# Kernel tuning notes

Measured on AMD Instinct MI355X. Metric: run time of the kernel, lower is better.

The kernel has to match this reference:

```python
import jax, jax.numpy as jnp
import numpy as np

B, HN, N1, N2, S = 32, 12, 256, 320, 256  # S = hardcoded 256 buffer size
EPS = 1e-5


def setup_inputs() -> dict:
    key = jax.random.key(0)
    ks = jax.random.split(key, 6)
    attn_rgb = jax.random.normal(ks[0], (B, HN, N1, N2), dtype=jnp.float32)
    attn_tir = jax.random.normal(ks[1], (B, HN, N1, N2), dtype=jnp.float32)
    # per-batch unique indices in [0, 256): permutation (collision-free scatter)
    perm = jax.vmap(lambda k: jax.random.permutation(k, S))(jax.random.split(ks[2], B))
    global_index_s = perm[:, :N1].astype(jnp.int32)
    # LayerNorm(512) params
    ln_g = jnp.ones((2 * S,), jnp.float32)
    ln_b = jnp.zeros((2 * S,), jnp.float32)
    # Linear(512,256) xavier-uniform weight, zero bias (stored as [in,out])
    lim1 = float(np.sqrt(6.0 / (2 * S + S)))
    W1 = jax.random.uniform(ks[3], (2 * S, S), jnp.float32, -lim1, lim1)
    b1 = jnp.zeros((S,), jnp.float32)
    # Linear(256,512)
    lim2 = float(np.sqrt(6.0 / (S + 2 * S)))
    W2 = jax.random.uniform(ks[4], (S, 2 * S), jnp.float32, -lim2, lim2)
    b2 = jnp.zeros((2 * S,), jnp.float32)
    return {"attn_rgb": attn_rgb, "attn_tir": attn_tir, "global_index_s": global_index_s,
            "ln_g": ln_g, "ln_b": ln_b, "W1": W1, "b1": b1, "W2": W2, "b2": b2}


def reference(attn_rgb, attn_tir, global_index_s, ln_g, ln_b, W1, b1, W2, b2):
    Bv, hn, n1, _ = attn_rgb.shape
    idx = jnp.broadcast_to(global_index_s[:, None, :].astype(jnp.int32), (Bv, hn, n1))  # [B,hn,N1]
    # detach() in torch source -> stop_gradient on the max-pooled path
    mx_rgb = jax.lax.stop_gradient(attn_rgb).max(-1)  # [B,hn,N1]
    mx_tir = jax.lax.stop_gradient(attn_tir).max(-1)
    bi = jnp.arange(Bv)[:, None, None]
    hi = jnp.arange(hn)[None, :, None]
    vex_rgb = jnp.zeros((Bv, hn, S), attn_rgb.dtype).at[bi, hi, idx].set(mx_rgb)
    vex_tir = jnp.zeros((Bv, hn, S), attn_tir.dtype).at[bi, hi, idx].set(mx_tir)
    v = jnp.concatenate([vex_rgb, vex_tir], axis=-1)  # [B,hn,512]
    # LayerNorm(512)
    mu = v.mean(-1, keepdims=True)
    var = v.var(-1, keepdims=True)
    v = (v - mu) * jax.lax.rsqrt(var + EPS) * ln_g + ln_b
    # SE MLP: Linear -> ReLU -> Linear -> Sigmoid
    h = jax.nn.relu(jnp.einsum('bhe,ef->bhf', v, W1) + b1)
    g = jax.nn.sigmoid(jnp.einsum('bhf,fe->bhe', h, W2) + b2)  # [B,hn,512]
    # gather gates back via indices and modulate
    g_rgb = jnp.take_along_axis(g[..., :S], idx, axis=-1)[..., None]  # [B,hn,N1,1]
    g_tir = jnp.take_along_axis(g[..., S:], idx, axis=-1)[..., None]
    attn_rgb_col = g_rgb * attn_rgb
    attn_tir_col = g_tir * attn_tir
    return (attn_tir_col, attn_rgb_col)
```

## Files before the change

### kernel.cpp

```cpp
#include <hip/hip_runtime.h>
#include <hip/hip_bf16.h>
#include <math.h>

#define BB   32
#define HN   12
#define N1   256
#define N2   320
#define SS   256
#define BH   (BB*HN)
#define R4   (N2/4)
#define SLICE4 ((size_t)N1*R4)

typedef float v4f __attribute__((ext_vector_type(4)));

__global__ __launch_bounds__(256, 2) void k_fused(
    const float* __restrict__ rgb, const float* __restrict__ tir,
    const int*   __restrict__ gidx,
    const float* __restrict__ ln_g, const float* __restrict__ ln_b,
    const float* __restrict__ W1,  const float* __restrict__ b1,
    const float* __restrict__ W2,  const float* __restrict__ b2,
    v4f* __restrict__ outTir, v4f* __restrict__ outRgb)
{
    __shared__ float mxs[2 * SS];
    __shared__ float v[2 * SS];
    __shared__ float hs[SS];
    __shared__ float gs[2 * SS];
    __shared__ float growR[SS];
    __shared__ float growT[SS];
    __shared__ int   sidx_s[SS];
    __shared__ float red[8];

    const int bh   = (int)blockIdx.x;
    const int b    = bh / HN;
    const int t    = (int)threadIdx.x;
    const int w    = t >> 6;
    const int lane = t & 63;

    sidx_s[t] = gidx[b * SS + t];
    v[t] = 0.f; v[t + SS] = 0.f;

    const v4f* srcR = (const v4f*)rgb + (size_t)bh * SLICE4;
    const v4f* srcT = (const v4f*)tir + (size_t)bh * SLICE4;

    for (int rr = 0; rr < 64; rr += 4) {
        const int r = w * 64 + rr;
        v4f aR[4], bRv[4], aT[4], bTv[4];
#pragma unroll
        for (int q = 0; q < 4; ++q) {
            const v4f* pR = srcR + (size_t)(r + q) * R4;
            const v4f* pT = srcT + (size_t)(r + q) * R4;
            aR[q]  = pR[lane];
            bRv[q] = pR[64 + (lane & 15)];
            aT[q]  = pT[lane];
            bTv[q] = pT[64 + (lane & 15)];
        }
#pragma unroll
        for (int q = 0; q < 4; ++q) {
            float mR = fmaxf(fmaxf(fmaxf(aR[q].x, aR[q].y), fmaxf(aR[q].z, aR[q].w)),
                             fmaxf(fmaxf(bRv[q].x, bRv[q].y), fmaxf(bRv[q].z, bRv[q].w)));
            float mT = fmaxf(fmaxf(fmaxf(aT[q].x, aT[q].y), fmaxf(aT[q].z, aT[q].w)),
                             fmaxf(fmaxf(bTv[q].x, bTv[q].y), fmaxf(bTv[q].z, bTv[q].w)));
#pragma unroll
            for (int off = 32; off; off >>= 1) {
                mR = fmaxf(mR, __shfl_xor(mR, off));
                mT = fmaxf(mT, __shfl_xor(mT, off));
            }
            if (lane == 0) { mxs[r + q] = mR; mxs[SS + r + q] = mT; }
        }
    }
    __syncthreads();

    {
        int sidx = sidx_s[t];
        v[sidx]      = mxs[t];
        v[sidx + SS] = mxs[SS + t];
    }
    __syncthreads();

    {
        float x0 = v[t], x1 = v[t + SS];
        float s  = x0 + x1;
        float sq = x0 * x0 + x1 * x1;
#pragma unroll
        for (int off = 32; off; off >>= 1) {
            s  += __shfl_xor(s, off);
            sq += __shfl_xor(sq, off);
        }
        if (lane == 0) { red[w] = s; red[4 + w] = sq; }
        __syncthreads();
        s  = red[0] + red[1] + red[2] + red[3];
        sq = red[4] + red[5] + red[6] + red[7];
        const float mu   = s * (1.f / 512.f);
        const float var  = sq * (1.f / 512.f) - mu * mu;
        const float rstd = rsqrtf(var + 1e-5f);
        v[t]      = (x0 - mu) * rstd * ln_g[t]      + ln_b[t];
        v[t + SS] = (x1 - mu) * rstd * ln_g[t + SS] + ln_b[t + SS];
    }
    __syncthreads();

    {
        float a0 = b1[t], a1 = 0.f;
#pragma unroll 8
        for (int e = 0; e < SS; ++e)       a0 = fmaf(v[e], W1[e * SS + t], a0);
#pragma unroll 8
        for (int e = SS; e < 2 * SS; ++e)  a1 = fmaf(v[e], W1[e * SS + t], a1);
        hs[t] = fmaxf(a0 + a1, 0.f);
    }
    __syncthreads();

    {
        float lo0 = b2[t], lo1 = 0.f, hi0 = b2[t + SS], hi1 = 0.f;
#pragma unroll 8
        for (int f = 0; f < 128; ++f) {
            float hv = hs[f];
            lo0 = fmaf(hv, W2[f * 2 * SS + t],      lo0);
            hi0 = fmaf(hv, W2[f * 2 * SS + t + SS], hi0);
        }
#pragma unroll 8
        for (int f = 128; f < SS; ++f) {
            float hv = hs[f];
            lo1 = fmaf(hv, W2[f * 2 * SS + t],      lo1);
            hi1 = fmaf(hv, W2[f * 2 * SS + t + SS], hi1);
        }
        gs[t]      = 1.f / (1.f + expf(-(lo0 + lo1)));
        gs[t + SS] = 1.f / (1.f + expf(-(hi0 + hi1)));
    }
    __syncthreads();

    growR[t] = gs[sidx_s[t]];
    growT[t] = gs[sidx_s[t] + SS];
    __syncthreads();

    {
        v4f* dstR = outRgb + (size_t)bh * SLICE4;
        v4f* dstT = outTir + (size_t)bh * SLICE4;
        for (int k = 0; k < 80; k += 8) {
            v4f aR[8], aT[8];
#pragma unroll
            for (int q = 0; q < 8; ++q) {
                unsigned i = (unsigned)(k + q) * 256u + (unsigned)t;
                aR[q] = srcR[i];
                aT[q] = srcT[i];
            }
#pragma unroll
            for (int q = 0; q < 8; ++q) {
                unsigned i   = (unsigned)(k + q) * 256u + (unsigned)t;
                unsigned row = i / 80u;
                v4f oR = aR[q] * growR[row];
                v4f oT = aT[q] * growT[row];
                __builtin_nontemporal_store(oT, dstT + i);
                __builtin_nontemporal_store(oR, dstR + i);
            }
        }
    }
}

extern "C" void kernel_launch(void* const* d_in, const int* in_sizes, int n_in,
                              void* d_out, int out_size, void* d_ws, size_t ws_size,
                              hipStream_t stream)
{
    const float* attn_rgb = (const float*)d_in[0];
    const float* attn_tir = (const float*)d_in[1];
    const int*   gidx     = (const int*)  d_in[2];
    const float* ln_g     = (const float*)d_in[3];
    const float* ln_b     = (const float*)d_in[4];
    const float* W1       = (const float*)d_in[5];
    const float* b1       = (const float*)d_in[6];
    const float* W2       = (const float*)d_in[7];
    const float* b2       = (const float*)d_in[8];

    v4f* outTir = (v4f*)d_out;
    v4f* outRgb = outTir + (size_t)BH * SLICE4;

    k_fused<<<BH, 256, 0, stream>>>(attn_rgb, attn_tir, gidx, ln_g, ln_b,
                                    W1, b1, W2, b2, outTir, outRgb);
}
```

Before: 138.9 us.

## Split fused kernel into rowmax, MLP, and modulate kernels for wider parallelism

Replaces the single per-(batch,head) fused kernel with three kernels: a grid-wide row-max reduction, a small per-(batch,head) LayerNorm+MLP kernel writing gate rows to workspace, and a wide elementwise modulation kernel. The goal is to fill the GPU with many more blocks during the two bandwidth-bound passes instead of 384 large blocks. It adds two kernel launches, a serial MLP stage between the passes, and workspace round-trips for maxima and gates.

```diff
diff --git a/kernel.cpp b/kernel.cpp
--- a/kernel.cpp
+++ b/kernel.cpp
@@ -8,25 +8,63 @@
 #define N2   320
 #define SS   256
 #define BH   (BB*HN)
+#define ROWS (BH*N1)
 #define R4   (N2/4)
-#define SLICE4 ((size_t)N1*R4)
+#define N4PT ((size_t)ROWS*R4)
 
 typedef float v4f __attribute__((ext_vector_type(4)));
 
-__global__ __launch_bounds__(256, 2) void k_fused(
+#define K1_BLOCKS 2048
+#define K1_WAVES  (K1_BLOCKS*4)
+#define ROWS_TOTAL (2*ROWS)
+#define RPW (ROWS_TOTAL/K1_WAVES)
+
+__global__ __launch_bounds__(256) void k_rowmax(
     const float* __restrict__ rgb, const float* __restrict__ tir,
+    float* __restrict__ mxr, float* __restrict__ mxt)
+{
+    const int gw   = ((int)blockIdx.x * 256 + (int)threadIdx.x) >> 6;
+    const int lane = threadIdx.x & 63;
+    const int base = gw * RPW;
+
+    for (int rr = 0; rr < RPW; rr += 4) {
+        v4f a[4], b[4];
+#pragma unroll
+        for (int q = 0; q < 4; ++q) {
+            int row   = base + rr + q;
+            int isTir = row >= ROWS;
+            int r     = isTir ? row - ROWS : row;
+            const v4f* p = (const v4f*)((isTir ? tir : rgb) + (size_t)r * N2);
+            a[q] = p[lane];
+            b[q] = p[64 + (lane & 15)];
+        }
+#pragma unroll
+        for (int q = 0; q < 4; ++q) {
+            float m = fmaxf(fmaxf(fmaxf(a[q].x, a[q].y), fmaxf(a[q].z, a[q].w)),
+                            fmaxf(fmaxf(b[q].x, b[q].y), fmaxf(b[q].z, b[q].w)));
+#pragma unroll
+            for (int off = 32; off; off >>= 1) m = fmaxf(m, __shfl_xor(m, off));
+            if (lane == 0) {
+                int row   = base + rr + q;
+                int isTir = row >= ROWS;
+                int r     = isTir ? row - ROWS : row;
+                (isTir ? mxt : mxr)[r] = m;
+            }
+        }
+    }
+}
+
+__global__ __launch_bounds__(256) void k_mlp(
     const int*   __restrict__ gidx,
+    const float* __restrict__ mxr, const float* __restrict__ mxt,
     const float* __restrict__ ln_g, const float* __restrict__ ln_b,
     const float* __restrict__ W1,  const float* __restrict__ b1,
     const float* __restrict__ W2,  const float* __restrict__ b2,
-    v4f* __restrict__ outTir, v4f* __restrict__ outRgb)
+    float* __restrict__ growR, float* __restrict__ growT)
 {
-    __shared__ float mxs[2 * SS];
     __shared__ float v[2 * SS];
     __shared__ float hs[SS];
     __shared__ float gs[2 * SS];
-    __shared__ float growR[SS];
-    __shared__ float growT[SS];
     __shared__ int   sidx_s[SS];
     __shared__ float red[8];
 
@@ -38,42 +76,12 @@
 
     sidx_s[t] = gidx[b * SS + t];
     v[t] = 0.f; v[t + SS] = 0.f;
-
-    const v4f* srcR = (const v4f*)rgb + (size_t)bh * SLICE4;
-    const v4f* srcT = (const v4f*)tir + (size_t)bh * SLICE4;
-
-    for (int rr = 0; rr < 64; rr += 4) {
-        const int r = w * 64 + rr;
-        v4f aR[4], bRv[4], aT[4], bTv[4];
-#pragma unroll
-        for (int q = 0; q < 4; ++q) {
-            const v4f* pR = srcR + (size_t)(r + q) * R4;
-            const v4f* pT = srcT + (size_t)(r + q) * R4;
-            aR[q]  = pR[lane];
-            bRv[q] = pR[64 + (lane & 15)];
-            aT[q]  = pT[lane];
-            bTv[q] = pT[64 + (lane & 15)];
-        }
-#pragma unroll
-        for (int q = 0; q < 4; ++q) {
-            float mR = fmaxf(fmaxf(fmaxf(aR[q].x, aR[q].y), fmaxf(aR[q].z, aR[q].w)),
-                             fmaxf(fmaxf(bRv[q].x, bRv[q].y), fmaxf(bRv[q].z, bRv[q].w)));
-            float mT = fmaxf(fmaxf(fmaxf(aT[q].x, aT[q].y), fmaxf(aT[q].z, aT[q].w)),
-                             fmaxf(fmaxf(bTv[q].x, bTv[q].y), fmaxf(bTv[q].z, bTv[q].w)));
-#pragma unroll
-            for (int off = 32; off; off >>= 1) {
-                mR = fmaxf(mR, __shfl_xor(mR, off));
-                mT = fmaxf(mT, __shfl_xor(mT, off));
-            }
-            if (lane == 0) { mxs[r + q] = mR; mxs[SS + r + q] = mT; }
-        }
-    }
     __syncthreads();
 
     {
         int sidx = sidx_s[t];
-        v[sidx]      = mxs[t];
-        v[sidx + SS] = mxs[SS + t];
+        v[sidx]      = mxr[bh * N1 + t];
+        v[sidx + SS] = mxt[bh * N1 + t];
     }
     __syncthreads();
 
@@ -127,32 +135,35 @@
     }
     __syncthreads();
 
-    growR[t] = gs[sidx_s[t]];
-    growT[t] = gs[sidx_s[t] + SS];
-    __syncthreads();
+    growR[bh * N1 + t] = gs[sidx_s[t]];
+    growT[bh * N1 + t] = gs[sidx_s[t] + SS];
+}
 
-    {
-        v4f* dstR = outRgb + (size_t)bh * SLICE4;
-        v4f* dstT = outTir + (size_t)bh * SLICE4;
-        for (int k = 0; k < 80; k += 8) {
-            v4f aR[8], aT[8];
+#define K3_HALF 3840
+#define K3_BLOCKS (2*K3_HALF)
+
+__global__ __launch_bounds__(256) void k_mod(
+    const float* __restrict__ rgb, const float* __restrict__ tir,
+    const float* __restrict__ growR, const float* __restrict__ growT,
+    v4f* __restrict__ outTir, v4f* __restrict__ outRgb)
+{
+    const int blk   = (int)blockIdx.x;
+    const int isRgb = blk >= K3_HALF;
+    const v4f*   src  = (const v4f*)(isRgb ? rgb : tir);
+    const float* grow = isRgb ? growR : growT;
+    v4f*         dst  = isRgb ? outRgb : outTir;
+
+    const unsigned j0 = (unsigned)(isRgb ? blk - K3_HALF : blk) * 2048u
+                      + (unsigned)threadIdx.x;
+    v4f a[8];
 #pragma unroll
-            for (int q = 0; q < 8; ++q) {
-                unsigned i = (unsigned)(k + q) * 256u + (unsigned)t;
-                aR[q] = srcR[i];
-                aT[q] = srcT[i];
-            }
+    for (int q = 0; q < 8; ++q) a[q] = src[j0 + q * 256u];
+    float g[8];
 #pragma unroll
-            for (int q = 0; q < 8; ++q) {
-                unsigned i   = (unsigned)(k + q) * 256u + (unsigned)t;
-                unsigned row = i / 80u;
-                v4f oR = aR[q] * growR[row];
-                v4f oT = aT[q] * growT[row];
-                __builtin_nontemporal_store(oT, dstT + i);
-                __builtin_nontemporal_store(oR, dstR + i);
-            }
-        }
-    }
+    for (int q = 0; q < 8; ++q) g[q] = grow[(j0 + q * 256u) / 80u];
+#pragma unroll
+    for (int q = 0; q < 8; ++q)
+        __builtin_nontemporal_store(a[q] * g[q], &dst[j0 + q * 256u]);
 }
 
 extern "C" void kernel_launch(void* const* d_in, const int* in_sizes, int n_in,
@@ -169,9 +180,20 @@
     const float* W2       = (const float*)d_in[7];
     const float* b2       = (const float*)d_in[8];
 
+    float* ws    = (float*)d_ws;
+    float* mxr   = ws;
+    float* mxt   = mxr + ROWS;
+    float* growR = mxt + ROWS;
+    float* growT = growR + ROWS;
+
     v4f* outTir = (v4f*)d_out;
-    v4f* outRgb = outTir + (size_t)BH * SLICE4;
+    v4f* outRgb = outTir + N4PT;
 
-    k_fused<<<BH, 256, 0, stream>>>(attn_rgb, attn_tir, gidx, ln_g, ln_b,
-                                    W1, b1, W2, b2, outTir, outRgb);
+    k_rowmax<<<K1_BLOCKS, 256, 0, stream>>>(attn_rgb, attn_tir, mxr, mxt);
+
+    k_mlp<<<BH, 256, 0, stream>>>(gidx, mxr, mxt, ln_g, ln_b,
+                                  W1, b1, W2, b2, growR, growT);
+
+    k_mod<<<K3_BLOCKS, 256, 0, stream>>>(attn_rgb, attn_tir, growR, growT,
+                                         outTir, outRgb);
 }
```

Result: slower. 170.1 us (+22.5%).

## Double block size to 512 threads and redistribute all phases across them

Applied to the files above, without the earlier changes.

Launches 512 threads per (batch, head) block instead of 256 and remaps every phase so each thread handles one element. The max-reduce covers rgb and tir rows as a single 512-row range, LayerNorm uses one value per thread, W1 is split into two input halves reduced through shared memory, and W2 gives each thread one output. The final modulate streams both tensors in one flat index space. The aim is more in-flight memory requests per block on this bandwidth-bound kernel, at the cost of an extra barrier and per-element select logic.

```diff
diff --git a/kernel.cpp b/kernel.cpp
--- a/kernel.cpp
+++ b/kernel.cpp
@@ -13,7 +13,7 @@
 
 typedef float v4f __attribute__((ext_vector_type(4)));
 
-__global__ __launch_bounds__(256, 2) void k_fused(
+__global__ __launch_bounds__(512, 4) void k_fused(
     const float* __restrict__ rgb, const float* __restrict__ tir,
     const int*   __restrict__ gidx,
     const float* __restrict__ ln_g, const float* __restrict__ ln_b,
@@ -23,12 +23,13 @@
 {
     __shared__ float mxs[2 * SS];
     __shared__ float v[2 * SS];
+    __shared__ float h2[2][SS];
     __shared__ float hs[SS];
     __shared__ float gs[2 * SS];
     __shared__ float growR[SS];
     __shared__ float growT[SS];
     __shared__ int   sidx_s[SS];
-    __shared__ float red[8];
+    __shared__ float red[16];
 
     const int bh   = (int)blockIdx.x;
     const int b    = bh / HN;
@@ -36,120 +37,116 @@
     const int w    = t >> 6;
     const int lane = t & 63;
 
-    sidx_s[t] = gidx[b * SS + t];
-    v[t] = 0.f; v[t + SS] = 0.f;
+    if (t < SS) sidx_s[t] = gidx[b * SS + t];
+    v[t] = 0.f;
 
-    const v4f* srcR = (const v4f*)rgb + (size_t)bh * SLICE4;
-    const v4f* srcT = (const v4f*)tir + (size_t)bh * SLICE4;
+    const float* sliceR = rgb + (size_t)bh * SLICE4 * 4;
+    const float* sliceT = tir + (size_t)bh * SLICE4 * 4;
 
-    for (int rr = 0; rr < 64; rr += 4) {
-        const int r = w * 64 + rr;
-        v4f aR[4], bRv[4], aT[4], bTv[4];
+    for (int uu = 0; uu < 64; uu += 8) {
+        const int u0 = w * 64 + uu;
+        v4f a[8], b8[8];
 #pragma unroll
-        for (int q = 0; q < 4; ++q) {
-            const v4f* pR = srcR + (size_t)(r + q) * R4;
-            const v4f* pT = srcT + (size_t)(r + q) * R4;
-            aR[q]  = pR[lane];
-            bRv[q] = pR[64 + (lane & 15)];
-            aT[q]  = pT[lane];
-            bTv[q] = pT[64 + (lane & 15)];
+        for (int q = 0; q < 8; ++q) {
+            int u   = u0 + q;
+            int row = u & 255;
+            const v4f* p = (const v4f*)((u >= SS ? sliceT : sliceR)
+                                        + (size_t)row * N2);
+            a[q]  = p[lane];
+            b8[q] = p[64 + (lane & 15)];
         }
 #pragma unroll
-        for (int q = 0; q < 4; ++q) {
-            float mR = fmaxf(fmaxf(fmaxf(aR[q].x, aR[q].y), fmaxf(aR[q].z, aR[q].w)),
-                             fmaxf(fmaxf(bRv[q].x, bRv[q].y), fmaxf(bRv[q].z, bRv[q].w)));
-            float mT = fmaxf(fmaxf(fmaxf(aT[q].x, aT[q].y), fmaxf(aT[q].z, aT[q].w)),
-                             fmaxf(fmaxf(bTv[q].x, bTv[q].y), fmaxf(bTv[q].z, bTv[q].w)));
+        for (int q = 0; q < 8; ++q) {
+            float m = fmaxf(fmaxf(fmaxf(a[q].x, a[q].y), fmaxf(a[q].z, a[q].w)),
+                            fmaxf(fmaxf(b8[q].x, b8[q].y), fmaxf(b8[q].z, b8[q].w)));
 #pragma unroll
-            for (int off = 32; off; off >>= 1) {
-                mR = fmaxf(mR, __shfl_xor(mR, off));
-                mT = fmaxf(mT, __shfl_xor(mT, off));
-            }
-            if (lane == 0) { mxs[r + q] = mR; mxs[SS + r + q] = mT; }
+            for (int off = 32; off; off >>= 1) m = fmaxf(m, __shfl_xor(m, off));
+            if (lane == 0) mxs[u0 + q] = m;
         }
     }
     __syncthreads();
 
-    {
+    if (t < SS) {
         int sidx = sidx_s[t];
         v[sidx]      = mxs[t];
-        v[sidx + SS] = mxs[SS + t];
+        v[sidx + SS] = mxs[t + SS];
     }
     __syncthreads();
 
     {
-        float x0 = v[t], x1 = v[t + SS];
-        float s  = x0 + x1;
-        float sq = x0 * x0 + x1 * x1;
+        float x  = v[t];
+        float s  = x;
+        float sq = x * x;
 #pragma unroll
         for (int off = 32; off; off >>= 1) {
             s  += __shfl_xor(s, off);
             sq += __shfl_xor(sq, off);
         }
-        if (lane == 0) { red[w] = s; red[4 + w] = sq; }
+        if (lane == 0) { red[w] = s; red[8 + w] = sq; }
         __syncthreads();
-        s  = red[0] + red[1] + red[2] + red[3];
-        sq = red[4] + red[5] + red[6] + red[7];
+        s  = red[0] + red[1] + red[2] + red[3] + red[4] + red[5] + red[6] + red[7];
+        sq = red[8] + red[9] + red[10] + red[11] + red[12] + red[13] + red[14] + red[15];
         const float mu   = s * (1.f / 512.f);
         const float var  = sq * (1.f / 512.f) - mu * mu;
         const float rstd = rsqrtf(var + 1e-5f);
-        v[t]      = (x0 - mu) * rstd * ln_g[t]      + ln_b[t];
-        v[t + SS] = (x1 - mu) * rstd * ln_g[t + SS] + ln_b[t + SS];
+        v[t] = (x - mu) * rstd * ln_g[t] + ln_b[t];
     }
     __syncthreads();
 
     {
-        float a0 = b1[t], a1 = 0.f;
+        const int out = t & 255, seg = t >> 8;
+        const int e0  = seg * SS;
+        float a0 = (seg == 0) ? b1[out] : 0.f, a1 = 0.f;
 #pragma unroll 8
-        for (int e = 0; e < SS; ++e)       a0 = fmaf(v[e], W1[e * SS + t], a0);
+        for (int e = 0; e < 128; ++e)
+            a0 = fmaf(v[e0 + e],       W1[(e0 + e) * SS + out],       a0);
 #pragma unroll 8
-        for (int e = SS; e < 2 * SS; ++e)  a1 = fmaf(v[e], W1[e * SS + t], a1);
-        hs[t] = fmaxf(a0 + a1, 0.f);
+        for (int e = 128; e < 256; ++e)
+            a1 = fmaf(v[e0 + e],       W1[(e0 + e) * SS + out],       a1);
+        h2[seg][out] = a0 + a1;
+    }
+    __syncthreads();
+    if (t < SS) hs[t] = fmaxf(h2[0][t] + h2[1][t], 0.f);
+    __syncthreads();
+
+    {
+        float a0 = b2[t], a1 = 0.f;
+#pragma unroll 8
+        for (int f = 0; f < 128; ++f)      a0 = fmaf(hs[f], W2[f * 2 * SS + t], a0);
+#pragma unroll 8
+        for (int f = 128; f < 256; ++f)    a1 = fmaf(hs[f], W2[f * 2 * SS + t], a1);
+        gs[t] = 1.f / (1.f + expf(-(a0 + a1)));
+    }
+    __syncthreads();
+
+    if (t < SS) {
+        growR[t] = gs[sidx_s[t]];
+        growT[t] = gs[sidx_s[t] + SS];
     }
     __syncthreads();
 
     {
-        float lo0 = b2[t], lo1 = 0.f, hi0 = b2[t + SS], hi1 = 0.f;
-#pragma unroll 8
-        for (int f = 0; f < 128; ++f) {
-            float hv = hs[f];
-            lo0 = fmaf(hv, W2[f * 2 * SS + t],      lo0);
-            hi0 = fmaf(hv, W2[f * 2 * SS + t + SS], hi0);
-        }
-#pragma unroll 8
-        for (int f = 128; f < SS; ++f) {
-            float hv = hs[f];
-            lo1 = fmaf(hv, W2[f * 2 * SS + t],      lo1);
-            hi1 = fmaf(hv, W2[f * 2 * SS + t + SS], hi1);
-        }
-        gs[t]      = 1.f / (1.f + expf(-(lo0 + lo1)));
-        gs[t + SS] = 1.f / (1.f + expf(-(hi0 + hi1)));
-    }
-    __syncthreads();
-
-    growR[t] = gs[sidx_s[t]];
-    growT[t] = gs[sidx_s[t] + SS];
-    __syncthreads();
-
-    {
+        const v4f* srcR4 = (const v4f*)sliceR;
+        const v4f* srcT4 = (const v4f*)sliceT;
         v4f* dstR = outRgb + (size_t)bh * SLICE4;
         v4f* dstT = outTir + (size_t)bh * SLICE4;
         for (int k = 0; k < 80; k += 8) {
-            v4f aR[8], aT[8];
+            v4f a[8]; float g[8];
 #pragma unroll
             for (int q = 0; q < 8; ++q) {
-                unsigned i = (unsigned)(k + q) * 256u + (unsigned)t;
-                aR[q] = srcR[i];
-                aT[q] = srcT[i];
+                unsigned i = (unsigned)(k + q) * 512u + (unsigned)t;
+                int isRgb  = i >= 20480u;
+                unsigned j = isRgb ? i - 20480u : i;
+                a[q] = isRgb ? srcR4[j] : srcT4[j];
+                g[q] = (isRgb ? growR : growT)[j / 80u];
             }
 #pragma unroll
             for (int q = 0; q < 8; ++q) {
-                unsigned i   = (unsigned)(k + q) * 256u + (unsigned)t;
-                unsigned row = i / 80u;
-                v4f oR = aR[q] * growR[row];
-                v4f oT = aT[q] * growT[row];
-                __builtin_nontemporal_store(oT, dstT + i);
-                __builtin_nontemporal_store(oR, dstR + i);
+                unsigned i = (unsigned)(k + q) * 512u + (unsigned)t;
+                int isRgb  = i >= 20480u;
+                unsigned j = isRgb ? i - 20480u : i;
+                __builtin_nontemporal_store(a[q] * g[q],
+                                            (isRgb ? dstR : dstT) + j);
             }
         }
     }
@@ -172,6 +169,6 @@
     v4f* outTir = (v4f*)d_out;
     v4f* outRgb = outTir + (size_t)BH * SLICE4;
 
-    k_fused<<<BH, 256, 0, stream>>>(attn_rgb, attn_tir, gidx, ln_g, ln_b,
+    k_fused<<<BH, 512, 0, stream>>>(attn_rgb, attn_tir, gidx, ln_g, ln_b,
                                     W1, b1, W2, b2, outTir, outRgb);
 }
```

Measured after the change: 134.3 us. 1.03x faster.

## Split each head slice across two cooperating blocks with global flag handoff

Applied to the files above, without the earlier changes.

Each (batch, head) slice is now handled by two blocks, each covering half the rows. Both blocks compute row maxima and publish them to workspace, then signal through an atomic flag. One block runs LayerNorm and the MLP and publishes gates through a second flag, while the other spins until the gates arrive; both then scale and stream their half of the output. The goal is to double the grid for better CU occupancy and bandwidth use. The cost is inter-block spin-waiting, which can deadlock if the partner block is never co-resident, plus an extra memset launch.

```diff
diff --git a/kernel.cpp b/kernel.cpp
--- a/kernel.cpp
+++ b/kernel.cpp
@@ -11,145 +11,188 @@
 #define R4   (N2/4)
 #define SLICE4 ((size_t)N1*R4)
 
+#define AGENT __HIP_MEMORY_SCOPE_AGENT
+
 typedef float v4f __attribute__((ext_vector_type(4)));
 
-__global__ __launch_bounds__(256, 2) void k_fused(
+__global__ __launch_bounds__(256, 3) void k_pair(
     const float* __restrict__ rgb, const float* __restrict__ tir,
     const int*   __restrict__ gidx,
     const float* __restrict__ ln_g, const float* __restrict__ ln_b,
     const float* __restrict__ W1,  const float* __restrict__ b1,
     const float* __restrict__ W2,  const float* __restrict__ b2,
+    unsigned* __restrict__ flagA, unsigned* __restrict__ flagB,
+    float* __restrict__ mx_g,
+    float* __restrict__ grow_g,
     v4f* __restrict__ outTir, v4f* __restrict__ outRgb)
 {
-    __shared__ float mxs[2 * SS];
     __shared__ float v[2 * SS];
     __shared__ float hs[SS];
     __shared__ float gs[2 * SS];
-    __shared__ float growR[SS];
-    __shared__ float growT[SS];
     __shared__ int   sidx_s[SS];
     __shared__ float red[8];
-
-    const int bh   = (int)blockIdx.x;
+    __shared__ float growR[128];
+    __shared__ float growT[128];
+
+    const int j    = (int)blockIdx.x;
+    const int bh   = j >> 1;
+    const int half = j & 1;
     const int b    = bh / HN;
     const int t    = (int)threadIdx.x;
     const int w    = t >> 6;
     const int lane = t & 63;
-
-    sidx_s[t] = gidx[b * SS + t];
-    v[t] = 0.f; v[t + SS] = 0.f;
-
-    const v4f* srcR = (const v4f*)rgb + (size_t)bh * SLICE4;
-    const v4f* srcT = (const v4f*)tir + (size_t)bh * SLICE4;
-
-    for (int rr = 0; rr < 64; rr += 4) {
-        const int r = w * 64 + rr;
-        v4f aR[4], bRv[4], aT[4], bTv[4];
-#pragma unroll
-        for (int q = 0; q < 4; ++q) {
-            const v4f* pR = srcR + (size_t)(r + q) * R4;
-            const v4f* pT = srcT + (size_t)(r + q) * R4;
-            aR[q]  = pR[lane];
-            bRv[q] = pR[64 + (lane & 15)];
-            aT[q]  = pT[lane];
-            bTv[q] = pT[64 + (lane & 15)];
-        }
-#pragma unroll
-        for (int q = 0; q < 4; ++q) {
-            float mR = fmaxf(fmaxf(fmaxf(aR[q].x, aR[q].y), fmaxf(aR[q].z, aR[q].w)),
-                             fmaxf(fmaxf(bRv[q].x, bRv[q].y), fmaxf(bRv[q].z, bRv[q].w)));
-            float mT = fmaxf(fmaxf(fmaxf(aT[q].x, aT[q].y), fmaxf(aT[q].z, aT[q].w)),
-                             fmaxf(fmaxf(bTv[q].x, bTv[q].y), fmaxf(bTv[q].z, bTv[q].w)));
-#pragma unroll
-            for (int off = 32; off; off >>= 1) {
-                mR = fmaxf(mR, __shfl_xor(mR, off));
-                mT = fmaxf(mT, __shfl_xor(mT, off));
-            }
-            if (lane == 0) { mxs[r + q] = mR; mxs[SS + r + q] = mT; }
+    const int row0 = half * 128;
+
+    const float* sliceR = rgb + (size_t)bh * (N1 * N2);
+    const float* sliceT = tir + (size_t)bh * (N1 * N2);
+
+    {
+        float* mxout = mx_g + bh * 512;
+        for (int uu = 0; uu < 64; uu += 8) {
+            const int u0 = w * 64 + uu;
+            v4f a[8], b8[8];
+#pragma unroll
+            for (int q = 0; q < 8; ++q) {
+                int u   = u0 + q;
+                int row = row0 + (u & 127);
+                const v4f* p = (const v4f*)((u >= 128 ? sliceT : sliceR)
+                                            + (size_t)row * N2);
+                a[q]  = p[lane];
+                b8[q] = p[64 + (lane & 15)];
+            }
+#pragma unroll
+            for (int q = 0; q < 8; ++q) {
+                float m = fmaxf(fmaxf(fmaxf(a[q].x, a[q].y), fmaxf(a[q].z, a[q].w)),
+                                fmaxf(fmaxf(b8[q].x, b8[q].y), fmaxf(b8[q].z, b8[q].w)));
+#pragma unroll
+                for (int off = 32; off; off >>= 1) m = fmaxf(m, __shfl_xor(m, off));
+                if (lane == 0) {
+                    int u = u0 + q;
+                    __hip_atomic_store(&mxout[(u >> 7) * 256 + row0 + (u & 127)],
+                                       m, __ATOMIC_RELAXED, AGENT);
+                }
+            }
         }
     }
     __syncthreads();
+    if (t == 0) __hip_atomic_fetch_add(&flagA[bh], 1u, __ATOMIC_RELEASE, AGENT);
+
+    if (half == 0) {
+        if (t == 0) {
+            while (__hip_atomic_load(&flagA[bh], __ATOMIC_RELAXED, AGENT) < 2u)
+                __builtin_amdgcn_s_sleep(4);
+            (void)__hip_atomic_load(&flagA[bh], __ATOMIC_ACQUIRE, AGENT);
+        }
+        __syncthreads();
+
+        sidx_s[t] = gidx[b * SS + t];
+        float mR = __hip_atomic_load(&mx_g[bh * 512 + t],       __ATOMIC_RELAXED, AGENT);
+        float mT = __hip_atomic_load(&mx_g[bh * 512 + 256 + t], __ATOMIC_RELAXED, AGENT);
+        v[t] = 0.f; v[t + SS] = 0.f;
+        __syncthreads();
+        v[sidx_s[t]]      = mR;
+        v[sidx_s[t] + SS] = mT;
+        __syncthreads();
+
+        {
+            float x0 = v[t], x1 = v[t + SS];
+            float s  = x0 + x1;
+            float sq = x0 * x0 + x1 * x1;
+#pragma unroll
+            for (int off = 32; off; off >>= 1) {
+                s  += __shfl_xor(s, off);
+                sq += __shfl_xor(sq, off);
+            }
+            if (lane == 0) { red[w] = s; red[4 + w] = sq; }
+            __syncthreads();
+            s  = red[0] + red[1] + red[2] + red[3];
+            sq = red[4] + red[5] + red[6] + red[7];
+            const float mu   = s * (1.f / 512.f);
+            const float var  = sq * (1.f / 512.f) - mu * mu;
+            const float rstd = rsqrtf(var + 1e-5f);
+            v[t]      = (x0 - mu) * rstd * ln_g[t]      + ln_b[t];
+            v[t + SS] = (x1 - mu) * rstd * ln_g[t + SS] + ln_b[t + SS];
+        }
+        __syncthreads();
+
+        {
+            float a0 = b1[t], a1 = 0.f;
+#pragma unroll 8
+            for (int e = 0; e < SS; ++e)       a0 = fmaf(v[e], W1[e * SS + t], a0);
+#pragma unroll 8
+            for (int e = SS; e < 2 * SS; ++e)  a1 = fmaf(v[e], W1[e * SS + t], a1);
+            hs[t] = fmaxf(a0 + a1, 0.f);
+        }
+        __syncthreads();
+
+        {
+            float lo0 = b2[t], lo1 = 0.f, hi0 = b2[t + SS], hi1 = 0.f;
+#pragma unroll 8
+            for (int f = 0; f < 128; ++f) {
+                float hv = hs[f];
+                lo0 = fmaf(hv, W2[f * 2 * SS + t],      lo0);
+                hi0 = fmaf(hv, W2[f * 2 * SS + t + SS], hi0);
+            }
+#pragma unroll 8
+            for (int f = 128; f < SS; ++f) {
+                float hv = hs[f];
+                lo1 = fmaf(hv, W2[f * 2 * SS + t],      lo1);
+                hi1 = fmaf(hv, W2[f * 2 * SS + t + SS], hi1);
+            }
+            gs[t]      = 1.f / (1.f + expf(-(lo0 + lo1)));
+            gs[t + SS] = 1.f / (1.f + expf(-(hi0 + hi1)));
+        }
+        __syncthreads();
+
+        {
+            int s = sidx_s[t];
+            float gR = gs[s], gT = gs[s + SS];
+            if (t < 128) { growR[t] = gR; growT[t] = gT; }
+            else {
+                __hip_atomic_store(&grow_g[bh * 256 + (t - 128)],       gR,
+                                   __ATOMIC_RELAXED, AGENT);
+                __hip_atomic_store(&grow_g[bh * 256 + 128 + (t - 128)], gT,
+                                   __ATOMIC_RELAXED, AGENT);
+            }
+        }
+        __syncthreads();
+        if (t == 0) __hip_atomic_fetch_add(&flagB[bh], 1u, __ATOMIC_RELEASE, AGENT);
+    } else {
+        if (t == 0) {
+            while (__hip_atomic_load(&flagB[bh], __ATOMIC_RELAXED, AGENT) < 1u)
+                __builtin_amdgcn_s_sleep(4);
+            (void)__hip_atomic_load(&flagB[bh], __ATOMIC_ACQUIRE, AGENT);
+        }
+        __syncthreads();
+        if (t < 128) {
+            growR[t] = __hip_atomic_load(&grow_g[bh * 256 + t],       __ATOMIC_RELAXED, AGENT);
+            growT[t] = __hip_atomic_load(&grow_g[bh * 256 + 128 + t], __ATOMIC_RELAXED, AGENT);
+        }
+        __syncthreads();
+    }
 
     {
-        int sidx = sidx_s[t];
-        v[sidx]      = mxs[t];
-        v[sidx + SS] = mxs[SS + t];
-    }
-    __syncthreads();
-
-    {
-        float x0 = v[t], x1 = v[t + SS];
-        float s  = x0 + x1;
-        float sq = x0 * x0 + x1 * x1;
-#pragma unroll
-        for (int off = 32; off; off >>= 1) {
-            s  += __shfl_xor(s, off);
-            sq += __shfl_xor(sq, off);
-        }
-        if (lane == 0) { red[w] = s; red[4 + w] = sq; }
-        __syncthreads();
-        s  = red[0] + red[1] + red[2] + red[3];
-        sq = red[4] + red[5] + red[6] + red[7];
-        const float mu   = s * (1.f / 512.f);
-        const float var  = sq * (1.f / 512.f) - mu * mu;
-        const float rstd = rsqrtf(var + 1e-5f);
-        v[t]      = (x0 - mu) * rstd * ln_g[t]      + ln_b[t];
-        v[t + SS] = (x1 - mu) * rstd * ln_g[t + SS] + ln_b[t + SS];
-    }
-    __syncthreads();
-
-    {
-        float a0 = b1[t], a1 = 0.f;
-#pragma unroll 8
-        for (int e = 0; e < SS; ++e)       a0 = fmaf(v[e], W1[e * SS + t], a0);
-#pragma unroll 8
-        for (int e = SS; e < 2 * SS; ++e)  a1 = fmaf(v[e], W1[e * SS + t], a1);
-        hs[t] = fmaxf(a0 + a1, 0.f);
-    }
-    __syncthreads();
-
-    {
-        float lo0 = b2[t], lo1 = 0.f, hi0 = b2[t + SS], hi1 = 0.f;
-#pragma unroll 8
-        for (int f = 0; f < 128; ++f) {
-            float hv = hs[f];
-            lo0 = fmaf(hv, W2[f * 2 * SS + t],      lo0);
-            hi0 = fmaf(hv, W2[f * 2 * SS + t + SS], hi0);
-        }
-#pragma unroll 8
-        for (int f = 128; f < SS; ++f) {
-            float hv = hs[f];
-            lo1 = fmaf(hv, W2[f * 2 * SS + t],      lo1);
-            hi1 = fmaf(hv, W2[f * 2 * SS + t + SS], hi1);
-        }
-        gs[t]      = 1.f / (1.f + expf(-(lo0 + lo1)));
-        gs[t + SS] = 1.f / (1.f + expf(-(hi0 + hi1)));
-    }
-    __syncthreads();
-
-    growR[t] = gs[sidx_s[t]];
-    growT[t] = gs[sidx_s[t] + SS];
-    __syncthreads();
-
-    {
-        v4f* dstR = outRgb + (size_t)bh * SLICE4;
-        v4f* dstT = outTir + (size_t)bh * SLICE4;
-        for (int k = 0; k < 80; k += 8) {
-            v4f aR[8], aT[8];
-#pragma unroll
-            for (int q = 0; q < 8; ++q) {
-                unsigned i = (unsigned)(k + q) * 256u + (unsigned)t;
-                aR[q] = srcR[i];
-                aT[q] = srcT[i];
-            }
-#pragma unroll
-            for (int q = 0; q < 8; ++q) {
-                unsigned i   = (unsigned)(k + q) * 256u + (unsigned)t;
-                unsigned row = i / 80u;
-                v4f oR = aR[q] * growR[row];
-                v4f oT = aT[q] * growT[row];
-                __builtin_nontemporal_store(oT, dstT + i);
-                __builtin_nontemporal_store(oR, dstR + i);
+        const v4f* sR4 = (const v4f*)sliceR;
+        const v4f* sT4 = (const v4f*)sliceT;
+        v4f* dR = outRgb + (size_t)bh * SLICE4;
+        v4f* dT = outTir + (size_t)bh * SLICE4;
+        const unsigned base = (unsigned)row0 * 80u;
+        for (int k = 0; k < 40; k += 8) {
+            v4f aR[8], aT[8]; float gR[8], gT[8];
+#pragma unroll
+            for (int q = 0; q < 8; ++q) {
+                unsigned i = base + (unsigned)(k + q) * 256u + (unsigned)t;
+                aR[q] = sR4[i];
+                aT[q] = sT4[i];
+                unsigned lr = (i / 80u) - (unsigned)row0;
+                gR[q] = growR[lr];
+                gT[q] = growT[lr];
+            }
+#pragma unroll
+            for (int q = 0; q < 8; ++q) {
+                unsigned i = base + (unsigned)(k + q) * 256u + (unsigned)t;
+                __builtin_nontemporal_store(aT[q] * gT[q], dT + i);
+                __builtin_nontemporal_store(aR[q] * gR[q], dR + i);
             }
         }
     }
@@ -169,9 +212,17 @@
     const float* W2       = (const float*)d_in[7];
     const float* b2       = (const float*)d_in[8];
 
+    unsigned* flagA = (unsigned*)d_ws;
+    unsigned* flagB = (unsigned*)((char*)d_ws + 4096);
+    float*    mx_g  = (float*)((char*)d_ws + 8192);
+    float*    grow_g = mx_g + (size_t)BH * 512;
+
     v4f* outTir = (v4f*)d_out;
     v4f* outRgb = outTir + (size_t)BH * SLICE4;
 
-    k_fused<<<BH, 256, 0, stream>>>(attn_rgb, attn_tir, gidx, ln_g, ln_b,
-                                    W1, b1, W2, b2, outTir, outRgb);
+    hipMemsetAsync(d_ws, 0, 8192, stream);
+
+    k_pair<<<2 * BH, 256, 0, stream>>>(attn_rgb, attn_tir, gidx, ln_g, ln_b,
+                                       W1, b1, W2, b2, flagA, flagB,
+                                       mx_g, grow_g, outTir, outRgb);
 }
```

After: 186.4 us. 1.34x slower.
